# Kernel tuning notes

Hardware: AMD Instinct MI355X
Metric: run time of the kernel (lower is better)

## Reference

```python
import jax, jax.numpy as jnp
import numpy as np

E = 256   # embed_dim
H = 8     # num_heads
D = E // H  # head_dim = 32
L = 1024  # seq len (Q_len == K_len == V_len)


def setup_inputs() -> dict:
    key = jax.random.key(0)
    ks = jax.random.split(key, 10)
    f = lambda k, s: jax.random.normal(k, s, dtype=jnp.float32)
    return {
        "V": f(ks[0], (L, E)),
        "K": f(ks[1], (L, E)),
        "Q": f(ks[2], (L, E)),
        # genomic-style coordinates, strictly positive
        "position": jax.random.uniform(ks[3], (L,), dtype=jnp.float32) * 1e5,
        "Wq": f(ks[4], (E, E)) * 0.02,
        "Wk": f(ks[5], (E, E)) * 0.02,
        "Wv": f(ks[6], (E, E)) * 0.02,
        "Wr": f(ks[7], (E, 1)) * 0.02,   # K_relative_linear weight [out=E, in=1]
        "Wo": f(ks[8], (E, E)) * 0.02,
        "bo": jnp.zeros((E,), jnp.float32),
    }


def reference(V, K, Q, position, Wq, Wk, Wv, Wr, Wo, bo):
    Lq = Q.shape[0]
    # projections (nn.Linear: x @ W.T), split into heads -> (L, H, D)
    q = (Q @ Wq.T).reshape(Lq, H, D)
    k = (K @ Wk.T).reshape(Lq, H, D)
    v = (V @ Wv.T).reshape(Lq, H, D)

    # relative position scalar per (q, k) pair: log(|p_q - p_k| + 1)
    rel = jnp.log(jnp.abs(position[:, None] - position[None, :]) + 1.0)  # (L, L)

    # K_relative_linear maps scalar rel -> (H, D); the einsum
    # 'nqhd,nhqjd->nhqj' then factorizes exactly as:
    #   sum_d Q[q,h,d] * rel[q,j] * Wr[h,d] = (Q . Wr)[h,q] * rel[q,j]
    # so we avoid materializing the (H, L, L, D) tensor while computing
    # mathematically identical results.
    Wr_h = Wr[:, 0].reshape(H, D)                    # (H, D)
    coeff = jnp.einsum('qhd,hd->hq', q, Wr_h)        # (H, L)

    energy = jnp.einsum('qhd,khd->hqk', q, k)        # (H, L, L)
    energy = energy + coeff[:, :, None] * rel[None, :, :]

    attn = jax.nn.softmax(energy / np.float32(E) ** 0.5, axis=2)
    out = jnp.einsum('hqk,khd->qhd', attn, v).reshape(Lq, E)
    out = out @ Wo.T + bo
    return out
```

## Files before the change

### kernel.cpp

```cpp
#include <hip/hip_runtime.h>
#include <math.h>

#define EDIM 256
#define LDIM 1024
#define HDIM 8
#define DDIM 32

typedef __attribute__((ext_vector_type(8))) short short8;
typedef __attribute__((ext_vector_type(4))) float f32x4;
typedef __attribute__((ext_vector_type(4))) unsigned u32x4;

__device__ inline unsigned short bf16h(float x) {
    unsigned u = __float_as_uint(x);
    return (unsigned short)((u + 0x7fff + ((u >> 16) & 1)) >> 16);
}
__device__ inline float bf16tof(unsigned short h) {
    return __uint_as_float(((unsigned)h) << 16);
}
__device__ inline unsigned packsplit(float x) {
    unsigned u = __float_as_uint(x);
    float r = x - __uint_as_float(u & 0xffff0000u);
    return (u & 0xffff0000u) | (unsigned)bf16h(r);
}

__global__ __launch_bounds__(256) void proj_kernel(
    const float* __restrict__ Q, const float* __restrict__ Km, const float* __restrict__ V,
    const float* __restrict__ Wq, const float* __restrict__ Wk, const float* __restrict__ Wv,
    const float* __restrict__ Wr,
    float* __restrict__ qT, float* __restrict__ kT, float* __restrict__ vT,
    float* __restrict__ coeff)
{
    const int z = blockIdx.z;
    const float* __restrict__ X = (z == 0) ? Q : (z == 1) ? Km : V;
    const float* __restrict__ W = (z == 0) ? Wq : (z == 1) ? Wk : Wv;
    float* __restrict__ dst     = (z == 0) ? qT : (z == 1) ? kT : vT;

    const int n0 = blockIdx.x * 32;
    const int o0 = blockIdx.y * 32;
    const int tid = threadIdx.x;
    const int tx = tid & 15, ty = tid >> 4;

    __shared__ float Xs[32][34];
    __shared__ float Ws[32][34];

    float acc[2][2] = {{0.f,0.f},{0.f,0.f}};

    const int sn  = tid >> 3;
    const int sc4 = (tid & 7) * 4;

    float4 xa = *(const float4*)(X + (n0 + sn) * EDIM + sc4);
    float4 wa = *(const float4*)(W + (o0 + sn) * EDIM + sc4);

    for (int kb = 0; kb < EDIM; kb += 32) {
        __syncthreads();
        Xs[sc4+0][sn]=xa.x; Xs[sc4+1][sn]=xa.y; Xs[sc4+2][sn]=xa.z; Xs[sc4+3][sn]=xa.w;
        Ws[sc4+0][sn]=wa.x; Ws[sc4+1][sn]=wa.y; Ws[sc4+2][sn]=wa.z; Ws[sc4+3][sn]=wa.w;
        float4 xn, wn;
        if (kb + 32 < EDIM) {
            xn = *(const float4*)(X + (n0 + sn) * EDIM + kb + 32 + sc4);
            wn = *(const float4*)(W + (o0 + sn) * EDIM + kb + 32 + sc4);
        }
        __syncthreads();
        #pragma unroll
        for (int e = 0; e < 32; ++e) {
            float2 x2 = *(const float2*)&Xs[e][ty*2];
            float2 w2 = *(const float2*)&Ws[e][tx*2];
            acc[0][0] += x2.x*w2.x; acc[0][1] += x2.x*w2.y;
            acc[1][0] += x2.y*w2.x; acc[1][1] += x2.y*w2.y;
        }
        xa = xn; wa = wn;
    }

    const int h = o0 >> 5;
    #pragma unroll
    for (int i = 0; i < 2; ++i) {
        const int n = n0 + ty*2 + i;
        float2 r; r.x = acc[i][0]; r.y = acc[i][1];
        *(float2*)(dst + h*(LDIM*DDIM) + n*DDIM + tx*2) = r;
    }

    if (z == 0) {
        const float wr0 = Wr[o0 + tx*2], wr1 = Wr[o0 + tx*2 + 1];
        #pragma unroll
        for (int i = 0; i < 2; ++i) {
            float c = acc[i][0]*wr0 + acc[i][1]*wr1;
            c += __shfl_xor(c, 1, 64);
            c += __shfl_xor(c, 2, 64);
            c += __shfl_xor(c, 4, 64);
            c += __shfl_xor(c, 8, 64);
            if (tx == 0) coeff[h*LDIM + n0 + ty*2 + i] = c;
        }
    }
}

__global__ __launch_bounds__(256, 4) void attn_kernel(
    const float* __restrict__ qT, const float* __restrict__ kT, const float* __restrict__ vT,
    const float* __restrict__ coeff, const float* __restrict__ pos,
    float* __restrict__ Op, float* __restrict__ Mp, float* __restrict__ Lp, int nkt)
{
    const int h   = blockIdx.y;
    const int q0  = blockIdx.x * 64;
    const int p   = blockIdx.z;
    const int kt0 = p * nkt * 64;
    const int tid  = threadIdx.x;
    const int wave = tid >> 6;
    const int lane = tid & 63;
    const int n    = lane & 15;
    const int quad = lane >> 4;
    const int qs0  = wave * 16;

    __shared__ __align__(16) short khi[4*64*8];
    __shared__ __align__(16) short klo[4*64*8];
    __shared__ __align__(16) unsigned vs2[32][68];
    __shared__ __align__(16) unsigned pA[64][68];
    __shared__ float pk[64];

    short8 qhi, qlo;
    {
        const float* qp = qT + (h*LDIM + q0 + qs0 + n) * DDIM + quad*8;
        float4 qa = *(const float4*)qp;
        float4 qb = *(const float4*)(qp + 4);
        float v[8] = {qa.x,qa.y,qa.z,qa.w, qb.x,qb.y,qb.z,qb.w};
        #pragma unroll
        for (int j = 0; j < 8; ++j) {
            unsigned u = __float_as_uint(v[j]);
            qhi[j] = (short)(u >> 16);
            qlo[j] = (short)bf16h(v[j] - __uint_as_float(u & 0xffff0000u));
        }
    }

    float pq[4], cq[4];
    #pragma unroll
    for (int i = 0; i < 4; ++i) {
        const int r = q0 + qs0 + 4*quad + i;
        pq[i] = pos[r];
        cq[i] = coeff[h*LDIM + r] * 0.0625f;
    }

    float m[4], l[4];
    #pragma unroll
    for (int i = 0; i < 4; ++i) { m[i] = -INFINITY; l[i] = 0.f; }

    f32x4 of0 = {0.f,0.f,0.f,0.f}, of1 = {0.f,0.f,0.f,0.f};

    const int cS = tid >> 2;
    const int dq = tid & 3;
    const int lane2 = (cS & 15) | (dq << 4);
    const int gS = cS >> 4;

    float4 k0c, k1c, v0c, v1c; float pkc = 0.f;
    {
        const float* kp = kT + (h*LDIM + kt0 + cS) * DDIM + dq*8;
        k0c = *(const float4*)kp; k1c = *(const float4*)(kp + 4);
        const float* vp = vT + (h*LDIM + kt0 + cS) * DDIM + dq*8;
        v0c = *(const float4*)vp; v1c = *(const float4*)(vp + 4);
        if (tid < 64) pkc = pos[kt0 + tid];
    }

    for (int t = 0; t < nkt; ++t) {
        __syncthreads();

        {
            float kv[8] = {k0c.x,k0c.y,k0c.z,k0c.w, k1c.x,k1c.y,k1c.z,k1c.w};
            short8 hi8, lo8;
            #pragma unroll
            for (int j = 0; j < 8; ++j) {
                unsigned u = __float_as_uint(kv[j]);
                hi8[j] = (short)(u >> 16);
                lo8[j] = (short)bf16h(kv[j] - __uint_as_float(u & 0xffff0000u));
            }
            *((short8*)&khi[(gS*64 + lane2)*8]) = hi8;
            *((short8*)&klo[(gS*64 + lane2)*8]) = lo8;
            float vv[8] = {v0c.x,v0c.y,v0c.z,v0c.w, v1c.x,v1c.y,v1c.z,v1c.w};
            #pragma unroll
            for (int j = 0; j < 8; ++j)
                vs2[dq*8 + j][cS] = packsplit(vv[j]);
            if (tid < 64) pk[tid] = pkc;
        }

        float4 k0n, k1n, v0n, v1n; float pkn = 0.f;
        if (t + 1 < nkt) {
            const int kt = kt0 + (t+1) * 64;
            const float* kp = kT + (h*LDIM + kt + cS) * DDIM + dq*8;
            k0n = *(const float4*)kp; k1n = *(const float4*)(kp + 4);
            const float* vp = vT + (h*LDIM + kt + cS) * DDIM + dq*8;
            v0n = *(const float4*)vp; v1n = *(const float4*)(vp + 4);
            if (tid < 64) pkn = pos[kt + tid];
        }
        __syncthreads();

        f32x4 Sf[4];
        #pragma unroll
        for (int t4 = 0; t4 < 4; ++t4) {
            short8 bhi = *((const short8*)&khi[(t4*64 + lane)*8]);
            short8 blo = *((const short8*)&klo[(t4*64 + lane)*8]);
            f32x4 acc = {0.f, 0.f, 0.f, 0.f};
            acc = __builtin_amdgcn_mfma_f32_16x16x32_bf16(qlo, bhi, acc, 0, 0, 0);
            acc = __builtin_amdgcn_mfma_f32_16x16x32_bf16(qhi, blo, acc, 0, 0, 0);
            acc = __builtin_amdgcn_mfma_f32_16x16x32_bf16(qhi, bhi, acc, 0, 0, 0);
            Sf[t4] = acc;
        }

        float ev[4][4];
        float rmax[4] = {-INFINITY, -INFINITY, -INFINITY, -INFINITY};
        #pragma unroll
        for (int t4 = 0; t4 < 4; ++t4) {
            const float pkt = pk[16*t4 + n];
            #pragma unroll
            for (int i = 0; i < 4; ++i) {
                float s = fmaf(Sf[t4][i], 0.0625f, cq[i] * __logf(fabsf(pq[i] - pkt) + 1.f));
                ev[t4][i] = s;
                rmax[i] = fmaxf(rmax[i], s);
            }
        }
        #pragma unroll
        for (int off = 1; off < 16; off <<= 1)
            #pragma unroll
            for (int i = 0; i < 4; ++i)
                rmax[i] = fmaxf(rmax[i], __shfl_xor(rmax[i], off, 64));

        float al[4], rsum[4];
        #pragma unroll
        for (int i = 0; i < 4; ++i) {
            const float mn = fmaxf(m[i], rmax[i]);
            al[i] = __expf(m[i] - mn);
            m[i] = mn;
            rsum[i] = 0.f;
        }
        #pragma unroll
        for (int t4 = 0; t4 < 4; ++t4)
            #pragma unroll
            for (int i = 0; i < 4; ++i) {
                float e = __expf(ev[t4][i] - m[i]);
                rsum[i] += e;
                pA[qs0 + 4*quad + i][16*t4 + n] = packsplit(e);
            }
        #pragma unroll
        for (int off = 1; off < 16; off <<= 1)
            #pragma unroll
            for (int i = 0; i < 4; ++i)
                rsum[i] += __shfl_xor(rsum[i], off, 64);
        #pragma unroll
        for (int i = 0; i < 4; ++i) l[i] = l[i]*al[i] + rsum[i];

        #pragma unroll
        for (int i = 0; i < 4; ++i) { of0[i] *= al[i]; of1[i] *= al[i]; }

        #pragma unroll
        for (int ch = 0; ch < 2; ++ch) {
            const unsigned* ap = &pA[qs0 + n][ch*32 + quad*8];
            u32x4 a0 = *(const u32x4*)ap;
            u32x4 a1 = *(const u32x4*)(ap + 4);
            short8 phi, plo;
            #pragma unroll
            for (int j = 0; j < 4; ++j) {
                phi[j]   = (short)(a0[j] >> 16);
                plo[j]   = (short)(a0[j] & 0xffffu);
                phi[j+4] = (short)(a1[j] >> 16);
                plo[j+4] = (short)(a1[j] & 0xffffu);
            }
            #pragma unroll
            for (int dt = 0; dt < 2; ++dt) {
                const unsigned* vp = &vs2[dt*16 + n][ch*32 + quad*8];
                u32x4 b0 = *(const u32x4*)vp;
                u32x4 b1 = *(const u32x4*)(vp + 4);
                short8 vhi, vlo;
                #pragma unroll
                for (int j = 0; j < 4; ++j) {
                    vhi[j]   = (short)(b0[j] >> 16);
                    vlo[j]   = (short)(b0[j] & 0xffffu);
                    vhi[j+4] = (short)(b1[j] >> 16);
                    vlo[j+4] = (short)(b1[j] & 0xffffu);
                }
                f32x4& of = dt ? of1 : of0;
                of = __builtin_amdgcn_mfma_f32_16x16x32_bf16(plo, vhi, of, 0, 0, 0);
                of = __builtin_amdgcn_mfma_f32_16x16x32_bf16(phi, vlo, of, 0, 0, 0);
                of = __builtin_amdgcn_mfma_f32_16x16x32_bf16(phi, vhi, of, 0, 0, 0);
            }
        }

        k0c = k0n; k1c = k1n; v0c = v0n; v1c = v1n; pkc = pkn;
    }

    const int ph = p * HDIM + h;
    {
        const size_t base = ((size_t)ph * LDIM + q0 + qs0) * DDIM;
        #pragma unroll
        for (int i = 0; i < 4; ++i) {
            Op[base + (size_t)(4*quad + i)*DDIM + n]      = of0[i];
            Op[base + (size_t)(4*quad + i)*DDIM + 16 + n] = of1[i];
        }
    }
    if (n == 0) {
        #pragma unroll
        for (int i = 0; i < 4; ++i) {
            const int r = q0 + qs0 + 4*quad + i;
            Mp[ph*LDIM + r] = m[i];
            Lp[ph*LDIM + r] = l[i];
        }
    }
}

__global__ __launch_bounds__(256) void combine_kernel(
    const float* __restrict__ Op, const float* __restrict__ Mp, const float* __restrict__ Lp,
    int P, float* __restrict__ A)
{
    const int idx = blockIdx.x * 256 + threadIdx.x;
    const int n  = idx >> 6;
    const int e4 = (idx & 63) * 4;
    const int h  = e4 >> 5;
    const int d  = e4 & 31;

    float mv[8], lv[8];
    float mx = -INFINITY;
    #pragma unroll
    for (int p = 0; p < 8; ++p) if (p < P) {
        mv[p] = Mp[(p*HDIM + h)*LDIM + n];
        lv[p] = Lp[(p*HDIM + h)*LDIM + n];
        mx = fmaxf(mx, mv[p]);
    }
    float s = 0.f;
    #pragma unroll
    for (int p = 0; p < 8; ++p) if (p < P) {
        float a = __expf(mv[p] - mx);
        mv[p] = a;
        s += a * lv[p];
    }
    const float inv = 1.f / s;

    float4 x; x.x = x.y = x.z = x.w = 0.f;
    #pragma unroll
    for (int p = 0; p < 8; ++p) if (p < P) {
        const float sp = mv[p] * inv;
        float4 xp = *(const float4*)(Op + ((size_t)(p*HDIM + h)*LDIM + n)*DDIM + d);
        x.x += sp*xp.x; x.y += sp*xp.y; x.z += sp*xp.z; x.w += sp*xp.w;
    }
    *(float4*)(A + n*EDIM + e4) = x;
}

__global__ __launch_bounds__(256) void outproj_kernel(
    const float* __restrict__ A, const float* __restrict__ Wo,
    const float* __restrict__ bo, float* __restrict__ out)
{
    const int n0 = blockIdx.x * 32;
    const int o0 = blockIdx.y * 32;
    const int tid = threadIdx.x;
    const int tx = tid & 15, ty = tid >> 4;

    __shared__ float Xs[32][34];
    __shared__ float Ws[32][34];

    float acc[2][2] = {{0.f,0.f},{0.f,0.f}};

    const int sn  = tid >> 3;
    const int sc4 = (tid & 7) * 4;

    float4 xa = *(const float4*)(A  + (n0 + sn) * EDIM + sc4);
    float4 wa = *(const float4*)(Wo + (o0 + sn) * EDIM + sc4);

    for (int kb = 0; kb < EDIM; kb += 32) {
        __syncthreads();
        Xs[sc4+0][sn]=xa.x; Xs[sc4+1][sn]=xa.y; Xs[sc4+2][sn]=xa.z; Xs[sc4+3][sn]=xa.w;
        Ws[sc4+0][sn]=wa.x; Ws[sc4+1][sn]=wa.y; Ws[sc4+2][sn]=wa.z; Ws[sc4+3][sn]=wa.w;
        float4 xn, wn;
        if (kb + 32 < EDIM) {
            xn = *(const float4*)(A  + (n0 + sn) * EDIM + kb + 32 + sc4);
            wn = *(const float4*)(Wo + (o0 + sn) * EDIM + kb + 32 + sc4);
        }
        __syncthreads();
        #pragma unroll
        for (int e = 0; e < 32; ++e) {
            float2 x2 = *(const float2*)&Xs[e][ty*2];
            float2 w2 = *(const float2*)&Ws[e][tx*2];
            acc[0][0] += x2.x*w2.x; acc[0][1] += x2.x*w2.y;
            acc[1][0] += x2.y*w2.x; acc[1][1] += x2.y*w2.y;
        }
        xa = xn; wa = wn;
    }

    const int oo = o0 + tx*2;
    float2 bias = *(const float2*)(bo + oo);
    #pragma unroll
    for (int i = 0; i < 2; ++i) {
        const int nn = n0 + ty*2 + i;
        float2 r; r.x = acc[i][0] + bias.x; r.y = acc[i][1] + bias.y;
        *(float2*)(out + nn*EDIM + oo) = r;
    }
}

extern "C" void kernel_launch(void* const* d_in, const int* in_sizes, int n_in,
                              void* d_out, int out_size, void* d_ws, size_t ws_size,
                              hipStream_t stream) {
    const float* V   = (const float*)d_in[0];
    const float* K   = (const float*)d_in[1];
    const float* Q   = (const float*)d_in[2];
    const float* pos = (const float*)d_in[3];
    const float* Wq  = (const float*)d_in[4];
    const float* Wk  = (const float*)d_in[5];
    const float* Wv  = (const float*)d_in[6];
    const float* Wr  = (const float*)d_in[7];
    const float* Wo  = (const float*)d_in[8];
    const float* bo  = (const float*)d_in[9];
    float* out = (float*)d_out;
    float* ws  = (float*)d_ws;

    auto need = [](int P) -> size_t {
        return (size_t)(794624 + P*278528) * 4;
    };
    int P = 2;
    if (ws_size >= need(8)) P = 8;
    else if (ws_size >= need(4)) P = 4;

    float* qT    = ws;
    float* kT    = ws + 262144;
    float* vT    = ws + 524288;
    float* coeff = ws + 786432;
    float* Op    = ws + 794624;
    float* Mp    = Op + (size_t)P * 262144;
    float* Lp    = Mp + (size_t)P * 8192;
    float* A     = qT;

    proj_kernel   <<<dim3(32, 8, 3), 256, 0, stream>>>(Q, K, V, Wq, Wk, Wv, Wr, qT, kT, vT, coeff);
    attn_kernel   <<<dim3(16, 8, P), 256, 0, stream>>>(qT, kT, vT, coeff, pos, Op, Mp, Lp, 16 / P);
    combine_kernel<<<dim3(256),      256, 0, stream>>>(Op, Mp, Lp, P, A);
    outproj_kernel<<<dim3(32, 8),    256, 0, stream>>>(A, Wo, bo, out);
}
```

Baseline: 117.7 us.

## Use split-bf16 MFMA for projections and pre-split Q/K/V in the projection kernel

The projection and output-projection GEMMs move from scalar FP32 FMA loops to 16x16x32 bf16 MFMA with a hi/lo split (three MFMAs per step) to keep near-FP32 accuracy. The projection kernel now writes Q/K/V already packed as hi|lo bf16 pairs, so the attention kernel no longer splits K and V in every tile iteration. The coeff reduction now needs an extra shared-memory step and a block sync. Rounding changes to round-to-nearest for the hi part, which slightly alters numerics.

```diff
diff --git a/kernel.cpp b/kernel.cpp
--- a/kernel.cpp
+++ b/kernel.cpp
@@ -22,79 +22,114 @@
     float r = x - __uint_as_float(u & 0xffff0000u);
     return (u & 0xffff0000u) | (unsigned)bf16h(r);
 }
+__device__ inline unsigned packsplit_rne(float x) {
+    unsigned short h = bf16h(x);
+    float r = x - bf16tof(h);
+    return ((unsigned)h << 16) | (unsigned)bf16h(r);
+}
 
 __global__ __launch_bounds__(256) void proj_kernel(
     const float* __restrict__ Q, const float* __restrict__ Km, const float* __restrict__ V,
     const float* __restrict__ Wq, const float* __restrict__ Wk, const float* __restrict__ Wv,
     const float* __restrict__ Wr,
-    float* __restrict__ qT, float* __restrict__ kT, float* __restrict__ vT,
+    unsigned* __restrict__ qT, unsigned* __restrict__ kT, unsigned* __restrict__ vT,
     float* __restrict__ coeff)
 {
     const int z = blockIdx.z;
     const float* __restrict__ X = (z == 0) ? Q : (z == 1) ? Km : V;
     const float* __restrict__ W = (z == 0) ? Wq : (z == 1) ? Wk : Wv;
-    float* __restrict__ dst     = (z == 0) ? qT : (z == 1) ? kT : vT;
+    unsigned* __restrict__ dst  = (z == 0) ? qT : (z == 1) ? kT : vT;
 
     const int n0 = blockIdx.x * 32;
     const int o0 = blockIdx.y * 32;
     const int tid = threadIdx.x;
-    const int tx = tid & 15, ty = tid >> 4;
-
-    __shared__ float Xs[32][34];
-    __shared__ float Ws[32][34];
-
-    float acc[2][2] = {{0.f,0.f},{0.f,0.f}};
-
-    const int sn  = tid >> 3;
-    const int sc4 = (tid & 7) * 4;
-
-    float4 xa = *(const float4*)(X + (n0 + sn) * EDIM + sc4);
-    float4 wa = *(const float4*)(W + (o0 + sn) * EDIM + sc4);
-
-    for (int kb = 0; kb < EDIM; kb += 32) {
-        __syncthreads();
-        Xs[sc4+0][sn]=xa.x; Xs[sc4+1][sn]=xa.y; Xs[sc4+2][sn]=xa.z; Xs[sc4+3][sn]=xa.w;
-        Ws[sc4+0][sn]=wa.x; Ws[sc4+1][sn]=wa.y; Ws[sc4+2][sn]=wa.z; Ws[sc4+3][sn]=wa.w;
-        float4 xn, wn;
-        if (kb + 32 < EDIM) {
-            xn = *(const float4*)(X + (n0 + sn) * EDIM + kb + 32 + sc4);
-            wn = *(const float4*)(W + (o0 + sn) * EDIM + kb + 32 + sc4);
-        }
-        __syncthreads();
-        #pragma unroll
-        for (int e = 0; e < 32; ++e) {
-            float2 x2 = *(const float2*)&Xs[e][ty*2];
-            float2 w2 = *(const float2*)&Ws[e][tx*2];
-            acc[0][0] += x2.x*w2.x; acc[0][1] += x2.x*w2.y;
-            acc[1][0] += x2.y*w2.x; acc[1][1] += x2.y*w2.y;
-        }
-        xa = xn; wa = wn;
-    }
-
-    const int h = o0 >> 5;
-    #pragma unroll
-    for (int i = 0; i < 2; ++i) {
-        const int n = n0 + ty*2 + i;
-        float2 r; r.x = acc[i][0]; r.y = acc[i][1];
-        *(float2*)(dst + h*(LDIM*DDIM) + n*DDIM + tx*2) = r;
+    const int wave = tid >> 6, lane = tid & 63;
+    const int n = lane & 15, quad = lane >> 4;
+    const int rh = wave & 1, oh = wave >> 1;
+
+    const int s    = tid >> 7;
+    const int r    = (tid >> 2) & 31;
+    const int qd   = tid & 3;
+    const int half = r >> 4;
+    const int fl8  = ((r & 15) | (qd << 4)) * 8;
+
+    __shared__ short Xhi[2][2][512], Xlo[2][2][512];
+    __shared__ short Whi[2][2][512], Wlo[2][2][512];
+    __shared__ float cpart[2][2][16];
+
+    const float* xp = X + (n0 + r) * EDIM + s * 32 + qd * 8;
+    const float* wp = W + (o0 + r) * EDIM + s * 32 + qd * 8;
+
+    float4 xa0 = *(const float4*)xp, xa1 = *(const float4*)(xp + 4);
+    float4 wa0 = *(const float4*)wp, wa1 = *(const float4*)(wp + 4);
+
+    f32x4 acc = {0.f, 0.f, 0.f, 0.f};
+
+    for (int kb = 0; kb < EDIM; kb += 64) {
+        __syncthreads();
+        {
+            float xv[8] = {xa0.x,xa0.y,xa0.z,xa0.w, xa1.x,xa1.y,xa1.z,xa1.w};
+            float wv[8] = {wa0.x,wa0.y,wa0.z,wa0.w, wa1.x,wa1.y,wa1.z,wa1.w};
+            short8 xh, xl, wh, wl;
+            #pragma unroll
+            for (int j = 0; j < 8; ++j) {
+                unsigned px = packsplit_rne(xv[j]);
+                unsigned pw = packsplit_rne(wv[j]);
+                xh[j] = (short)(px >> 16); xl[j] = (short)(px & 0xffffu);
+                wh[j] = (short)(pw >> 16); wl[j] = (short)(pw & 0xffffu);
+            }
+            *(short8*)&Xhi[s][half][fl8] = xh;
+            *(short8*)&Xlo[s][half][fl8] = xl;
+            *(short8*)&Whi[s][half][fl8] = wh;
+            *(short8*)&Wlo[s][half][fl8] = wl;
+        }
+        float4 xn0, xn1, wn0, wn1;
+        if (kb + 64 < EDIM) {
+            xn0 = *(const float4*)(xp + kb + 64); xn1 = *(const float4*)(xp + kb + 68);
+            wn0 = *(const float4*)(wp + kb + 64); wn1 = *(const float4*)(wp + kb + 68);
+        }
+        __syncthreads();
+        #pragma unroll
+        for (int ss = 0; ss < 2; ++ss) {
+            short8 ah = *(const short8*)&Xhi[ss][rh][lane*8];
+            short8 al = *(const short8*)&Xlo[ss][rh][lane*8];
+            short8 bh = *(const short8*)&Whi[ss][oh][lane*8];
+            short8 bl = *(const short8*)&Wlo[ss][oh][lane*8];
+            acc = __builtin_amdgcn_mfma_f32_16x16x32_bf16(al, bh, acc, 0, 0, 0);
+            acc = __builtin_amdgcn_mfma_f32_16x16x32_bf16(ah, bl, acc, 0, 0, 0);
+            acc = __builtin_amdgcn_mfma_f32_16x16x32_bf16(ah, bh, acc, 0, 0, 0);
+        }
+        xa0 = xn0; xa1 = xn1; wa0 = wn0; wa1 = wn1;
+    }
+
+    const int h  = o0 >> 5;
+    const int og = oh * 16 + n;
+    #pragma unroll
+    for (int i = 0; i < 4; ++i) {
+        const int row = rh * 16 + 4 * quad + i;
+        dst[(h * LDIM + n0 + row) * DDIM + og] = packsplit_rne(acc[i]);
     }
 
     if (z == 0) {
-        const float wr0 = Wr[o0 + tx*2], wr1 = Wr[o0 + tx*2 + 1];
-        #pragma unroll
-        for (int i = 0; i < 2; ++i) {
-            float c = acc[i][0]*wr0 + acc[i][1]*wr1;
+        const float wr = Wr[o0 + og];
+        #pragma unroll
+        for (int i = 0; i < 4; ++i) {
+            float c = acc[i] * wr;
             c += __shfl_xor(c, 1, 64);
             c += __shfl_xor(c, 2, 64);
             c += __shfl_xor(c, 4, 64);
             c += __shfl_xor(c, 8, 64);
-            if (tx == 0) coeff[h*LDIM + n0 + ty*2 + i] = c;
-        }
+            if (n == 0) cpart[rh][oh][4*quad + i] = c;
+        }
+        __syncthreads();
+        if (tid < 32)
+            coeff[h * LDIM + n0 + tid] = cpart[tid >> 4][0][tid & 15]
+                                       + cpart[tid >> 4][1][tid & 15];
     }
 }
 
 __global__ __launch_bounds__(256, 4) void attn_kernel(
-    const float* __restrict__ qT, const float* __restrict__ kT, const float* __restrict__ vT,
+    const unsigned* __restrict__ qT, const unsigned* __restrict__ kT, const unsigned* __restrict__ vT,
     const float* __restrict__ coeff, const float* __restrict__ pos,
     float* __restrict__ Op, float* __restrict__ Mp, float* __restrict__ Lp, int nkt)
 {
@@ -117,15 +152,13 @@
 
     short8 qhi, qlo;
     {
-        const float* qp = qT + (h*LDIM + q0 + qs0 + n) * DDIM + quad*8;
-        float4 qa = *(const float4*)qp;
-        float4 qb = *(const float4*)(qp + 4);
-        float v[8] = {qa.x,qa.y,qa.z,qa.w, qb.x,qb.y,qb.z,qb.w};
-        #pragma unroll
-        for (int j = 0; j < 8; ++j) {
-            unsigned u = __float_as_uint(v[j]);
-            qhi[j] = (short)(u >> 16);
-            qlo[j] = (short)bf16h(v[j] - __uint_as_float(u & 0xffff0000u));
+        const unsigned* qp = qT + (h*LDIM + q0 + qs0 + n) * DDIM + quad*8;
+        u32x4 a0 = *(const u32x4*)qp;
+        u32x4 a1 = *(const u32x4*)(qp + 4);
+        #pragma unroll
+        for (int j = 0; j < 4; ++j) {
+            qhi[j]   = (short)(a0[j] >> 16);  qlo[j]   = (short)(a0[j] & 0xffffu);
+            qhi[j+4] = (short)(a1[j] >> 16);  qlo[j+4] = (short)(a1[j] & 0xffffu);
         }
     }
 
@@ -148,12 +181,12 @@
     const int lane2 = (cS & 15) | (dq << 4);
     const int gS = cS >> 4;
 
-    float4 k0c, k1c, v0c, v1c; float pkc = 0.f;
+    u32x4 k0c, k1c, v0c, v1c; float pkc = 0.f;
     {
-        const float* kp = kT + (h*LDIM + kt0 + cS) * DDIM + dq*8;
-        k0c = *(const float4*)kp; k1c = *(const float4*)(kp + 4);
-        const float* vp = vT + (h*LDIM + kt0 + cS) * DDIM + dq*8;
-        v0c = *(const float4*)vp; v1c = *(const float4*)(vp + 4);
+        const unsigned* kp = kT + (h*LDIM + kt0 + cS) * DDIM + dq*8;
+        k0c = *(const u32x4*)kp; k1c = *(const u32x4*)(kp + 4);
+        const unsigned* vp = vT + (h*LDIM + kt0 + cS) * DDIM + dq*8;
+        v0c = *(const u32x4*)vp; v1c = *(const u32x4*)(vp + 4);
         if (tid < 64) pkc = pos[kt0 + tid];
     }
 
@@ -161,30 +194,29 @@
         __syncthreads();
 
         {
-            float kv[8] = {k0c.x,k0c.y,k0c.z,k0c.w, k1c.x,k1c.y,k1c.z,k1c.w};
             short8 hi8, lo8;
             #pragma unroll
-            for (int j = 0; j < 8; ++j) {
-                unsigned u = __float_as_uint(kv[j]);
-                hi8[j] = (short)(u >> 16);
-                lo8[j] = (short)bf16h(kv[j] - __uint_as_float(u & 0xffff0000u));
+            for (int j = 0; j < 4; ++j) {
+                hi8[j]   = (short)(k0c[j] >> 16);  lo8[j]   = (short)(k0c[j] & 0xffffu);
+                hi8[j+4] = (short)(k1c[j] >> 16);  lo8[j+4] = (short)(k1c[j] & 0xffffu);
             }
             *((short8*)&khi[(gS*64 + lane2)*8]) = hi8;
             *((short8*)&klo[(gS*64 + lane2)*8]) = lo8;
-            float vv[8] = {v0c.x,v0c.y,v0c.z,v0c.w, v1c.x,v1c.y,v1c.z,v1c.w};
-            #pragma unroll
-            for (int j = 0; j < 8; ++j)
-                vs2[dq*8 + j][cS] = packsplit(vv[j]);
+            #pragma unroll
+            for (int j = 0; j < 4; ++j) {
+                vs2[dq*8 + j][cS]     = v0c[j];
+                vs2[dq*8 + j + 4][cS] = v1c[j];
+            }
             if (tid < 64) pk[tid] = pkc;
         }
 
-        float4 k0n, k1n, v0n, v1n; float pkn = 0.f;
+        u32x4 k0n, k1n, v0n, v1n; float pkn = 0.f;
         if (t + 1 < nkt) {
             const int kt = kt0 + (t+1) * 64;
-            const float* kp = kT + (h*LDIM + kt + cS) * DDIM + dq*8;
-            k0n = *(const float4*)kp; k1n = *(const float4*)(kp + 4);
-            const float* vp = vT + (h*LDIM + kt + cS) * DDIM + dq*8;
-            v0n = *(const float4*)vp; v1n = *(const float4*)(vp + 4);
+            const unsigned* kp = kT + (h*LDIM + kt + cS) * DDIM + dq*8;
+            k0n = *(const u32x4*)kp; k1n = *(const u32x4*)(kp + 4);
+            const unsigned* vp = vT + (h*LDIM + kt + cS) * DDIM + dq*8;
+            v0n = *(const u32x4*)vp; v1n = *(const u32x4*)(vp + 4);
             if (tid < 64) pkn = pos[kt + tid];
         }
         __syncthreads();
@@ -345,46 +377,70 @@
     const int n0 = blockIdx.x * 32;
     const int o0 = blockIdx.y * 32;
     const int tid = threadIdx.x;
-    const int tx = tid & 15, ty = tid >> 4;
-
-    __shared__ float Xs[32][34];
-    __shared__ float Ws[32][34];
-
-    float acc[2][2] = {{0.f,0.f},{0.f,0.f}};
-
-    const int sn  = tid >> 3;
-    const int sc4 = (tid & 7) * 4;
-
-    float4 xa = *(const float4*)(A  + (n0 + sn) * EDIM + sc4);
-    float4 wa = *(const float4*)(Wo + (o0 + sn) * EDIM + sc4);
-
-    for (int kb = 0; kb < EDIM; kb += 32) {
-        __syncthreads();
-        Xs[sc4+0][sn]=xa.x; Xs[sc4+1][sn]=xa.y; Xs[sc4+2][sn]=xa.z; Xs[sc4+3][sn]=xa.w;
-        Ws[sc4+0][sn]=wa.x; Ws[sc4+1][sn]=wa.y; Ws[sc4+2][sn]=wa.z; Ws[sc4+3][sn]=wa.w;
-        float4 xn, wn;
-        if (kb + 32 < EDIM) {
-            xn = *(const float4*)(A  + (n0 + sn) * EDIM + kb + 32 + sc4);
-            wn = *(const float4*)(Wo + (o0 + sn) * EDIM + kb + 32 + sc4);
-        }
-        __syncthreads();
-        #pragma unroll
-        for (int e = 0; e < 32; ++e) {
-            float2 x2 = *(const float2*)&Xs[e][ty*2];
-            float2 w2 = *(const float2*)&Ws[e][tx*2];
-            acc[0][0] += x2.x*w2.x; acc[0][1] += x2.x*w2.y;
-            acc[1][0] += x2.y*w2.x; acc[1][1] += x2.y*w2.y;
-        }
-        xa = xn; wa = wn;
-    }
-
-    const int oo = o0 + tx*2;
-    float2 bias = *(const float2*)(bo + oo);
-    #pragma unroll
-    for (int i = 0; i < 2; ++i) {
-        const int nn = n0 + ty*2 + i;
-        float2 r; r.x = acc[i][0] + bias.x; r.y = acc[i][1] + bias.y;
-        *(float2*)(out + nn*EDIM + oo) = r;
+    const int wave = tid >> 6, lane = tid & 63;
+    const int n = lane & 15, quad = lane >> 4;
+    const int rh = wave & 1, oh = wave >> 1;
+
+    const int s    = tid >> 7;
+    const int r    = (tid >> 2) & 31;
+    const int qd   = tid & 3;
+    const int half = r >> 4;
+    const int fl8  = ((r & 15) | (qd << 4)) * 8;
+
+    __shared__ short Xhi[2][2][512], Xlo[2][2][512];
+    __shared__ short Whi[2][2][512], Wlo[2][2][512];
+
+    const float* xp = A  + (n0 + r) * EDIM + s * 32 + qd * 8;
+    const float* wp = Wo + (o0 + r) * EDIM + s * 32 + qd * 8;
+
+    float4 xa0 = *(const float4*)xp, xa1 = *(const float4*)(xp + 4);
+    float4 wa0 = *(const float4*)wp, wa1 = *(const float4*)(wp + 4);
+
+    f32x4 acc = {0.f, 0.f, 0.f, 0.f};
+
+    for (int kb = 0; kb < EDIM; kb += 64) {
+        __syncthreads();
+        {
+            float xv[8] = {xa0.x,xa0.y,xa0.z,xa0.w, xa1.x,xa1.y,xa1.z,xa1.w};
+            float wv[8] = {wa0.x,wa0.y,wa0.z,wa0.w, wa1.x,wa1.y,wa1.z,wa1.w};
+            short8 xh, xl, wh, wl;
+            #pragma unroll
+            for (int j = 0; j < 8; ++j) {
+                unsigned px = packsplit_rne(xv[j]);
+                unsigned pw = packsplit_rne(wv[j]);
+                xh[j] = (short)(px >> 16); xl[j] = (short)(px & 0xffffu);
+                wh[j] = (short)(pw >> 16); wl[j] = (short)(pw & 0xffffu);
+            }
+            *(short8*)&Xhi[s][half][fl8] = xh;
+            *(short8*)&Xlo[s][half][fl8] = xl;
+            *(short8*)&Whi[s][half][fl8] = wh;
+            *(short8*)&Wlo[s][half][fl8] = wl;
+        }
+        float4 xn0, xn1, wn0, wn1;
+        if (kb + 64 < EDIM) {
+            xn0 = *(const float4*)(xp + kb + 64); xn1 = *(const float4*)(xp + kb + 68);
+            wn0 = *(const float4*)(wp + kb + 64); wn1 = *(const float4*)(wp + kb + 68);
+        }
+        __syncthreads();
+        #pragma unroll
+        for (int ss = 0; ss < 2; ++ss) {
+            short8 ah = *(const short8*)&Xhi[ss][rh][lane*8];
+            short8 al = *(const short8*)&Xlo[ss][rh][lane*8];
+            short8 bh = *(const short8*)&Whi[ss][oh][lane*8];
+            short8 bl = *(const short8*)&Wlo[ss][oh][lane*8];
+            acc = __builtin_amdgcn_mfma_f32_16x16x32_bf16(al, bh, acc, 0, 0, 0);
+            acc = __builtin_amdgcn_mfma_f32_16x16x32_bf16(ah, bl, acc, 0, 0, 0);
+            acc = __builtin_amdgcn_mfma_f32_16x16x32_bf16(ah, bh, acc, 0, 0, 0);
+        }
+        xa0 = xn0; xa1 = xn1; wa0 = wn0; wa1 = wn1;
+    }
+
+    const int og = o0 + oh*16 + n;
+    const float b = bo[og];
+    #pragma unroll
+    for (int i = 0; i < 4; ++i) {
+        const int row = n0 + rh*16 + 4*quad + i;
+        out[row * EDIM + og] = acc[i] + b;
     }
 }
 
@@ -411,14 +467,14 @@
     if (ws_size >= need(8)) P = 8;
     else if (ws_size >= need(4)) P = 4;
 
-    float* qT    = ws;
-    float* kT    = ws + 262144;
-    float* vT    = ws + 524288;
+    unsigned* qT = (unsigned*)ws;
+    unsigned* kT = (unsigned*)(ws + 262144);
+    unsigned* vT = (unsigned*)(ws + 524288);
     float* coeff = ws + 786432;
     float* Op    = ws + 794624;
     float* Mp    = Op + (size_t)P * 262144;
     float* Lp    = Mp + (size_t)P * 8192;
-    float* A     = qT;
+    float* A     = ws;
 
     proj_kernel   <<<dim3(32, 8, 3), 256, 0, stream>>>(Q, K, V, Wq, Wk, Wv, Wr, qT, kT, vT, coeff);
     attn_kernel   <<<dim3(16, 8, P), 256, 0, stream>>>(qT, kT, vT, coeff, pos, Op, Mp, Lp, 16 / P);
```

New measurement: 106.8 us. 9.2% less time.
